# Optimization experiments

Hardware: AMD Instinct MI355X
Metric: run time of the kernel (lower is better)

## Reference

```python
import jax, jax.numpy as jnp
import numpy as np

CS = 128            # config.chunk_size
K = 8               # config.k + 1
EPS = 1e-6          # config.eps
L = K * CS          # extended_len = 1024


def setup_inputs() -> dict:
    key = jax.random.key(0)
    k1, k2 = jax.random.split(key)
    B, T, E = 2, 8192, 256
    x = jax.random.normal(k1, (B, T, E), dtype=jnp.float32)
    # xavier_normal_ on [CS, L]: std = sqrt(2 / (fan_in + fan_out))
    std = np.sqrt(2.0 / (CS + L)).astype(np.float32)
    down_proj = jax.random.normal(k2, (CS, L), dtype=jnp.float32) * std
    return {"x": x, "down_proj": down_proj}


def reference(x, down_proj):
    B, T, E = x.shape
    N = T // CS  # T chosen divisible by CS, so the pad branch is a no-op
    chunks = x.reshape(B, N, CS, E)

    # --- per-chunk retrieval scores (vectorized over the causal chunk loop) ---
    cn = chunks / (jnp.linalg.norm(chunks, axis=-1, keepdims=True) + EPS)
    # row-wise cosine sims between every pair of chunks: [B,N,N,CS,CS]
    sims = jnp.einsum('bice,bjde->bijcd', cn, cn)
    scores = sims.max(axis=-1).sum(axis=-1)              # [B,N,N]
    i_idx = jnp.arange(N)
    causal = i_idx[None, :] < i_idx[:, None]             # j < i allowed
    NEG = jnp.asarray(-1e9, x.dtype)
    scores = jnp.where(causal[None], scores, NEG)

    # --- topk selection, weights (num_sel_i = min(i, K-1)) ---
    vals, idx = jax.lax.top_k(scores, K - 1)             # descending, [B,N,K-1]
    num_sel = jnp.minimum(i_idx, K - 1)                  # [N]
    vmin_slot = jnp.clip(num_sel - 1, 0, K - 2)          # last valid slot = min of topk vals
    v_min = jnp.take_along_axis(vals, jnp.broadcast_to(vmin_slot[None, :, None], (B, N, 1)), axis=-1)
    slot = jnp.arange(K - 1)
    valid = slot[None, :] < num_sel[:, None]             # [N,K-1]
    w = jnp.where(valid[None], vals / (v_min + EPS), 0.0)  # [B,N,K-1]

    # --- weighted gather of selected chunks ---
    b_idx = jnp.arange(B)[:, None, None]
    sel = chunks[b_idx, idx]                             # [B,N,K-1,CS,E]
    weighted = sel * w[..., None, None]

    # --- left-pad to L: zeros occupy leftmost slots, then topk-ordered chunks, then cur ---
    shift = jnp.maximum(0, (K - 1) - i_idx)              # [N]
    src = jnp.clip(slot[None, :] - shift[:, None], 0, K - 2)   # [N,K-1]
    n_idx = jnp.arange(N)[None, :, None]
    arranged = weighted[b_idx, n_idx, src[None]]         # [B,N,K-1,CS,E]
    keep = slot[None, :] >= shift[:, None]
    arranged = jnp.where(keep[None, :, :, None, None], arranged, 0.0)

    ext = jnp.concatenate([arranged.reshape(B, N, (K - 1) * CS, E), chunks], axis=2)  # [B,N,L,E]
    # down_proj @ ext + x_chunks, then contract back to [B,T,E]
    out = jnp.einsum('cl,bnle->bnce', down_proj, ext) + chunks
    return out.reshape(B, N * CS, E)
```

## Files before the change

kernel.cpp:

```cpp
#include <hip/hip_runtime.h>
#include <hip/hip_bf16.h>

#define CS     128
#define EDIM   256
#define NBATCH 2
#define TLEN   8192
#define NCHUNK 64
#define LEXT   1024
#define KSEL   7

typedef __attribute__((ext_vector_type(8))) short   short8;
typedef __attribute__((ext_vector_type(4))) float   floatx4;

__device__ inline short bf16_of(float f) {
    __hip_bfloat16 h = __float2bfloat16(f);
    return *(short*)&h;
}
__device__ inline float f_of_bf16(short s) {
    __hip_bfloat16 h = *(__hip_bfloat16*)&s;
    return __bfloat162float(h);
}

__device__ inline void gl_lds16(const void* g, void* l) {
    __builtin_amdgcn_global_load_lds(
        (const __attribute__((address_space(1))) unsigned int*)g,
        (__attribute__((address_space(3))) unsigned int*)l, 16, 0, 0);
}

#define RAW_BAR() asm volatile("s_barrier" ::: "memory")

__global__ __launch_bounds__(256) void prep_kernel(const float* __restrict__ x,
                                                   const float* __restrict__ dp,
                                                   short* __restrict__ cn_hi,
                                                   short* __restrict__ cn_lo,
                                                   short* __restrict__ xt_hi,
                                                   short* __restrict__ dp_hi) {
    const int bx = blockIdx.x;
    if (bx >= 256) {
        int t = (bx - 256) * 256 + threadIdx.x;
#pragma unroll
        for (int u = 0; u < 16; ++u) {
            int idx = (t * 16 + u) * 4;
            float4 v = *(const float4*)(dp + idx);
            *(short4*)(dp_hi + idx) =
                make_short4(bf16_of(v.x), bf16_of(v.y), bf16_of(v.z), bf16_of(v.w));
        }
        return;
    }

    __shared__ float tile[64 * 257];
    const int b = bx >> 7, t0 = (bx & 127) * 64;
    const int tid = threadIdx.x;
    const int r = tid >> 2, q = tid & 3;

    const float* src = x + ((size_t)(b * TLEN + t0 + r)) * EDIM + q * 64;
    float* trow = &tile[r * 257 + q * 64];
    float s = 0.f;
#pragma unroll
    for (int u = 0; u < 16; ++u) {
        float4 v = *(const float4*)(src + u * 4);
        s += v.x * v.x + v.y * v.y + v.z * v.z + v.w * v.w;
        trow[u * 4 + 0] = v.x; trow[u * 4 + 1] = v.y;
        trow[u * 4 + 2] = v.z; trow[u * 4 + 3] = v.w;
    }
    s += __shfl_xor(s, 1);
    s += __shfl_xor(s, 2);
    const float rn = 1.0f / (sqrtf(s) + 1e-6f);

    short* ch = cn_hi + ((size_t)(b * TLEN + t0 + r)) * EDIM + q * 64;
    short* cl = cn_lo + ((size_t)(b * TLEN + t0 + r)) * EDIM + q * 64;
#pragma unroll
    for (int u = 0; u < 16; ++u) {
        short hs[4], ls[4];
#pragma unroll
        for (int k2 = 0; k2 < 4; ++k2) {
            float c = trow[u * 4 + k2] * rn;
            hs[k2] = bf16_of(c);
            ls[k2] = bf16_of(c - f_of_bf16(hs[k2]));
        }
        *(short4*)(ch + u * 4) = make_short4(hs[0], hs[1], hs[2], hs[3]);
        *(short4*)(cl + u * 4) = make_short4(ls[0], ls[1], ls[2], ls[3]);
    }
    __syncthreads();

    const int g16 = tid >> 4, tq = tid & 15;
#pragma unroll
    for (int it = 0; it < 16; ++it) {
        int e = g16 + it * 16;
        short hs2[4];
#pragma unroll
        for (int g = 0; g < 4; ++g)
            hs2[g] = bf16_of(tile[(tq * 4 + g) * 257 + e]);
        *(short4*)(xt_hi + ((size_t)(b * EDIM + e)) * TLEN + t0 + tq * 4)
            = make_short4(hs2[0], hs2[1], hs2[2], hs2[3]);
    }
}

__global__ __launch_bounds__(256) void scores_mfma(const short* __restrict__ cn_hi,
                                                   const short* __restrict__ cn_lo,
                                                   float* __restrict__ scores) {
    __shared__ short tiles[2][4][4096];
    double* red2   = (double*)&tiles[0][0][0];
    float*  redbuf = (float*)&tiles[0][0][8];

    const int p = blockIdx.x, b = blockIdx.y;
    int i = (int)((1.0f + sqrtf(1.0f + 8.0f * (float)p)) * 0.5f);
    while (i * (i - 1) / 2 > p) --i;
    while (i * (i + 1) / 2 <= p) ++i;
    const int j = p - i * (i - 1) / 2;

    const int tid  = threadIdx.x;
    const int w    = tid >> 6, lane = tid & 63;
    const int wr   = w >> 1, wc = w & 1;
    const int quad = lane >> 4, l15 = lane & 15;

    const short* sarr  = (w & 1) ? cn_lo : cn_hi;
    const size_t sbase = ((size_t)b * TLEN + ((w >> 1) ? j : i) * CS) * EDIM;
    const int rr  = lane >> 2;
    const int c16 = (lane & 3) * 8;
    const int csw = c16 ^ (((rr >> 1) & 3) * 8);
    const int q8  = (quad ^ ((l15 >> 1) & 3)) * 8;

    auto stage = [&](int ks, int bf) {
        const short* gsrc = sarr + sbase + ks * 32 + csw;
        short* ldst = &tiles[bf][w][0];
#pragma unroll
        for (int t = 0; t < 8; ++t)
            gl_lds16(gsrc + (size_t)(16 * t + rr) * EDIM, ldst + t * 512);
    };

    floatx4 acc[4][4];
#pragma unroll
    for (int rt = 0; rt < 4; ++rt)
#pragma unroll
        for (int ct = 0; ct < 4; ++ct) acc[rt][ct] = (floatx4){0.f, 0.f, 0.f, 0.f};

    stage(0, 0);
    int buf = 0;
    for (int ks = 0; ks < 8; ++ks) {
        if (ks < 7) {
            stage(ks + 1, buf ^ 1);
            asm volatile("s_waitcnt vmcnt(8)" ::: "memory");
        } else {
            asm volatile("s_waitcnt vmcnt(0)" ::: "memory");
        }
        RAW_BAR();

        short8 bh[4], bl[4];
#pragma unroll
        for (int ct = 0; ct < 4; ++ct) {
            int r = wc * 64 + ct * 16 + l15;
            bh[ct] = *(const short8*)&tiles[buf][2][r * 32 + q8];
            bl[ct] = *(const short8*)&tiles[buf][3][r * 32 + q8];
        }
        __builtin_amdgcn_s_setprio(1);
#pragma unroll
        for (int rt = 0; rt < 4; ++rt) {
            int r = wr * 64 + rt * 16 + l15;
            short8 ah = *(const short8*)&tiles[buf][0][r * 32 + q8];
            short8 al = *(const short8*)&tiles[buf][1][r * 32 + q8];
#pragma unroll
            for (int ct = 0; ct < 4; ++ct) {
                acc[rt][ct] = __builtin_amdgcn_mfma_f32_16x16x32_bf16(ah, bh[ct], acc[rt][ct], 0, 0, 0);
                acc[rt][ct] = __builtin_amdgcn_mfma_f32_16x16x32_bf16(ah, bl[ct], acc[rt][ct], 0, 0, 0);
                acc[rt][ct] = __builtin_amdgcn_mfma_f32_16x16x32_bf16(al, bh[ct], acc[rt][ct], 0, 0, 0);
            }
        }
        __builtin_amdgcn_s_setprio(0);
        RAW_BAR();
        buf ^= 1;
    }

#pragma unroll
    for (int rt = 0; rt < 4; ++rt) {
        float m[4];
#pragma unroll
        for (int reg = 0; reg < 4; ++reg) {
            float mm = acc[rt][0][reg];
#pragma unroll
            for (int ct = 1; ct < 4; ++ct) mm = fmaxf(mm, acc[rt][ct][reg]);
            m[reg] = mm;
        }
#pragma unroll
        for (int off = 1; off < 16; off <<= 1)
#pragma unroll
            for (int reg = 0; reg < 4; ++reg) m[reg] = fmaxf(m[reg], __shfl_xor(m[reg], off));
        if (l15 == 0) {
#pragma unroll
            for (int reg = 0; reg < 4; ++reg)
                redbuf[wc * 128 + wr * 64 + rt * 16 + quad * 4 + reg] = m[reg];
        }
    }
    __syncthreads();

    double part = 0.0;
    if (tid < 128) part = (double)fmaxf(redbuf[tid], redbuf[128 + tid]);
#pragma unroll
    for (int off = 1; off < 64; off <<= 1) part += __shfl_xor(part, off);
    if (lane == 0 && w < 2) red2[w] = part;
    __syncthreads();
    if (tid == 0) scores[(b * NCHUNK + i) * NCHUNK + j] = (float)(red2[0] + red2[1]);
}

__global__ __launch_bounds__(256) void out_mfma(const float* __restrict__ x,
                                                const short* __restrict__ dph,
                                                const short* __restrict__ xth,
                                                const float* __restrict__ scores,
                                                float* __restrict__ out) {
    __shared__ short As[2][128 * 32];
    __shared__ short Bs[2][64 * 32];
    __shared__ int   slist[8], sslot[8], snum;
    __shared__ float swei[8];

    const int eq = blockIdx.x, n = blockIdx.y, b = blockIdx.z;
    const int e0 = eq * 64;
    const int tid  = threadIdx.x;
    const int w    = tid >> 6, lane = tid & 63;
    const int wr   = w >> 1, wc = w & 1;
    const int quad = lane >> 4, l15 = lane & 15;
    const int rr   = lane >> 2;
    const int c16  = (lane & 3) * 8;
    const int csw  = c16 ^ (((rr >> 1) & 3) * 8);
    const int q8   = (quad ^ ((l15 >> 1) & 3)) * 8;

    if (w == 0) {
        const float* srow = scores + (b * NCHUNK + n) * NCHUNK;
        const int nsel = n < KSEL ? n : KSEL;
        float v = (lane < n) ? srow[lane] : -3.0e38f;
        float vals[KSEL];
        int   idxs[KSEL];
        for (int s2 = 0; s2 < nsel; ++s2) {
            float bv = v; int bi = lane;
#pragma unroll
            for (int off = 1; off < 64; off <<= 1) {
                float ov = __shfl_xor(bv, off);
                int   oi = __shfl_xor(bi, off);
                if (ov > bv || (ov == bv && oi < bi)) { bv = ov; bi = oi; }
            }
            vals[s2] = bv; idxs[s2] = bi;
            if (lane == bi) v = -3.0e38f;
        }
        if (lane == 0) {
            float vmin = (nsel > 0) ? vals[nsel - 1] : 0.0f;
            float inv  = 1.0f / (vmin + 1e-6f);
            int shift  = KSEL - nsel;
            int c = 0;
            for (int s2 = 0; s2 < 8; ++s2) {
                int jj; float ww;
                if (s2 < KSEL) {
                    int tt = s2 - shift;
                    if (tt >= 0) { jj = idxs[tt]; ww = vals[tt] * inv; }
                    else         { jj = -1;       ww = 0.0f; }
                } else { jj = n; ww = 1.0f; }
                if (jj >= 0) { slist[c] = jj; sslot[c] = s2; swei[c] = ww; ++c; }
            }
            snum = c;
        }
    }
    __syncthreads();
    const int NS = snum * 4;

    auto stage = [&](int st, int bf) {
        int sv = st >> 2, kk = st & 3;
        if (w < 2) {
            const short* gsrc = dph + (size_t)(sslot[sv] * 128 + kk * 32) + csw;
#pragma unroll
            for (int t = 0; t < 4; ++t)
                gl_lds16(gsrc + (size_t)(w * 64 + t * 16 + rr) * LEXT,
                         &As[bf][(w * 64 + t * 16) * 32]);
        } else {
            const short* gsrc = xth + ((size_t)(b * EDIM + e0)) * TLEN
                                + (size_t)(slist[sv] * CS + kk * 32) + csw;
#pragma unroll
            for (int t = 0; t < 2; ++t)
                gl_lds16(gsrc + (size_t)((w - 2) * 32 + t * 16 + rr) * TLEN,
                         &Bs[bf][((w - 2) * 32 + t * 16) * 32]);
        }
    };

    floatx4 accT[4][2], accP[4][2];
#pragma unroll
    for (int rt = 0; rt < 4; ++rt)
#pragma unroll
        for (int ct = 0; ct < 2; ++ct) accT[rt][ct] = (floatx4){0.f, 0.f, 0.f, 0.f};

    stage(0, 0);
    int buf = 0;
    for (int st = 0; st < NS; ++st) {
        if (st + 1 < NS) {
            stage(st + 1, buf ^ 1);
            if (w < 2) asm volatile("s_waitcnt vmcnt(4)" ::: "memory");
            else       asm volatile("s_waitcnt vmcnt(2)" ::: "memory");
        } else {
            asm volatile("s_waitcnt vmcnt(0)" ::: "memory");
        }
        RAW_BAR();

        if ((st & 3) == 0) {
#pragma unroll
            for (int rt = 0; rt < 4; ++rt)
#pragma unroll
                for (int ct = 0; ct < 2; ++ct) accP[rt][ct] = (floatx4){0.f, 0.f, 0.f, 0.f};
        }

        short8 bh[2];
#pragma unroll
        for (int ct = 0; ct < 2; ++ct) {
            int e = wc * 32 + ct * 16 + l15;
            bh[ct] = *(const short8*)&Bs[buf][e * 32 + q8];
        }
        __builtin_amdgcn_s_setprio(1);
#pragma unroll
        for (int rt = 0; rt < 4; ++rt) {
            int r = wr * 64 + rt * 16 + l15;
            short8 ah = *(const short8*)&As[buf][r * 32 + q8];
#pragma unroll
            for (int ct = 0; ct < 2; ++ct)
                accP[rt][ct] = __builtin_amdgcn_mfma_f32_16x16x32_bf16(ah, bh[ct], accP[rt][ct], 0, 0, 0);
        }
        __builtin_amdgcn_s_setprio(0);

        if ((st & 3) == 3) {
            float wcur = swei[st >> 2];
#pragma unroll
            for (int rt = 0; rt < 4; ++rt)
#pragma unroll
                for (int ct = 0; ct < 2; ++ct)
#pragma unroll
                    for (int reg = 0; reg < 4; ++reg)
                        accT[rt][ct][reg] += wcur * accP[rt][ct][reg];
        }
        RAW_BAR();
        buf ^= 1;
    }

#pragma unroll
    for (int rt = 0; rt < 4; ++rt)
#pragma unroll
        for (int ct = 0; ct < 2; ++ct) {
#pragma unroll
            for (int reg = 0; reg < 4; ++reg) {
                int row = wr * 64 + rt * 16 + quad * 4 + reg;
                int col = wc * 32 + ct * 16 + l15;
                size_t o = ((size_t)(b * TLEN + n * CS + row)) * EDIM + e0 + col;
                out[o] = accT[rt][ct][reg] + x[o];
            }
        }
}

extern "C" void kernel_launch(void* const* d_in, const int* in_sizes, int n_in,
                              void* d_out, int out_size, void* d_ws, size_t ws_size,
                              hipStream_t stream) {
    const float* x  = (const float*)d_in[0];
    const float* dp = (const float*)d_in[1];
    float* out = (float*)d_out;

    char* ws = (char*)d_ws;
    short* cn_hi  = (short*)(ws);
    short* cn_lo  = (short*)(ws + (8u << 20));
    short* xt_hi  = (short*)(ws + (16u << 20));
    short* dp_hi  = (short*)(ws + (24u << 20));
    float* scores = (float*)(ws + (25u << 20));

    prep_kernel <<<dim3(264), 256, 0, stream>>>(x, dp, cn_hi, cn_lo, xt_hi, dp_hi);
    scores_mfma <<<dim3(NCHUNK * (NCHUNK - 1) / 2, NBATCH), 256, 0, stream>>>(cn_hi, cn_lo, scores);
    out_mfma    <<<dim3(4, NCHUNK, NBATCH), 256, 0, stream>>>(x, dp_hi, xt_hi, scores, out);
}
```

Before: 203.2 us.

## Repack normalized chunks k-blocked, use 32x32 MFMA for scores, triple-buffer out GEMM

The prep kernel now writes the normalized hi/lo bf16 chunks in a k-slab-blocked layout, so the scores kernel can stage contiguous 16-wide K slices with fewer loads per stage. The scores kernel switches from 16x16x32 to 32x32x16 MFMA tiles, halves its LDS, and adds an occupancy hint of 4 blocks per SM. The row-max reduction is reworked to match the new accumulator layout. The output GEMM moves to a three-buffer pipeline that loads 64-wide K per stage with one barrier per step, cutting barrier and wait overhead at the cost of more LDS.

New measurement: 208.3 us. 2.5% more time.

```diff
diff --git a/kernel.cpp b/kernel.cpp
--- a/kernel.cpp
+++ b/kernel.cpp
@@ -9,8 +9,9 @@
 #define LEXT   1024
 #define KSEL   7
 
-typedef __attribute__((ext_vector_type(8))) short   short8;
-typedef __attribute__((ext_vector_type(4))) float   floatx4;
+typedef __attribute__((ext_vector_type(8)))  short short8;
+typedef __attribute__((ext_vector_type(4)))  float floatx4;
+typedef __attribute__((ext_vector_type(16))) float floatx16;
 
 __device__ inline short bf16_of(float f) {
     __hip_bfloat16 h = __float2bfloat16(f);
@@ -49,6 +50,7 @@
     }
 
     __shared__ float tile[64 * 257];
+    __shared__ float rnbuf[64];
     const int b = bx >> 7, t0 = (bx & 127) * 64;
     const int tid = threadIdx.x;
     const int r = tid >> 2, q = tid & 3;
@@ -66,21 +68,7 @@
     s += __shfl_xor(s, 1);
     s += __shfl_xor(s, 2);
     const float rn = 1.0f / (sqrtf(s) + 1e-6f);
-
-    short* ch = cn_hi + ((size_t)(b * TLEN + t0 + r)) * EDIM + q * 64;
-    short* cl = cn_lo + ((size_t)(b * TLEN + t0 + r)) * EDIM + q * 64;
-#pragma unroll
-    for (int u = 0; u < 16; ++u) {
-        short hs[4], ls[4];
-#pragma unroll
-        for (int k2 = 0; k2 < 4; ++k2) {
-            float c = trow[u * 4 + k2] * rn;
-            hs[k2] = bf16_of(c);
-            ls[k2] = bf16_of(c - f_of_bf16(hs[k2]));
-        }
-        *(short4*)(ch + u * 4) = make_short4(hs[0], hs[1], hs[2], hs[3]);
-        *(short4*)(cl + u * 4) = make_short4(ls[0], ls[1], ls[2], ls[3]);
-    }
+    if (q == 0) rnbuf[r] = rn;
     __syncthreads();
 
     const int g16 = tid >> 4, tq = tid & 15;
@@ -94,12 +82,35 @@
         *(short4*)(xt_hi + ((size_t)(b * EDIM + e)) * TLEN + t0 + tq * 4)
             = make_short4(hs2[0], hs2[1], hs2[2], hs2[3]);
     }
-}
-
-__global__ __launch_bounds__(256) void scores_mfma(const short* __restrict__ cn_hi,
-                                                   const short* __restrict__ cn_lo,
-                                                   float* __restrict__ scores) {
-    __shared__ short tiles[2][4][4096];
+
+    const int chunk = t0 >> 7, half = (t0 >> 6) & 1;
+    const size_t cbase = ((size_t)(b * 64 + chunk)) * 32768 + (size_t)half * 1024;
+    const int ks = tid >> 4, l16 = tid & 15;
+#pragma unroll
+    for (int rr = 0; rr < 4; ++rr) {
+        int lrow = rr * 16 + l16;
+        float rnv = rnbuf[lrow];
+        short8 h0, h1, l0, l1;
+#pragma unroll
+        for (int k2 = 0; k2 < 16; ++k2) {
+            float c = tile[lrow * 257 + ks * 16 + k2] * rnv;
+            short hh = bf16_of(c);
+            short ll = bf16_of(c - f_of_bf16(hh));
+            if (k2 < 8) { h0[k2] = hh; l0[k2] = ll; }
+            else        { h1[k2 - 8] = hh; l1[k2 - 8] = ll; }
+        }
+        size_t o = cbase + (size_t)ks * 2048 + (size_t)lrow * 16;
+        *(short8*)(cn_hi + o)     = h0;
+        *(short8*)(cn_hi + o + 8) = h1;
+        *(short8*)(cn_lo + o)     = l0;
+        *(short8*)(cn_lo + o + 8) = l1;
+    }
+}
+
+__global__ __launch_bounds__(256, 4) void scores_mfma(const short* __restrict__ cn_hi,
+                                                      const short* __restrict__ cn_lo,
+                                                      float* __restrict__ scores) {
+    __shared__ short tiles[2][4][2048];
     double* red2   = (double*)&tiles[0][0][0];
     float*  redbuf = (float*)&tiles[0][0][8];
 
@@ -112,58 +123,57 @@
     const int tid  = threadIdx.x;
     const int w    = tid >> 6, lane = tid & 63;
     const int wr   = w >> 1, wc = w & 1;
-    const int quad = lane >> 4, l15 = lane & 15;
+    const int hi   = lane >> 5, l31 = lane & 31;
 
     const short* sarr  = (w & 1) ? cn_lo : cn_hi;
-    const size_t sbase = ((size_t)b * TLEN + ((w >> 1) ? j : i) * CS) * EDIM;
-    const int rr  = lane >> 2;
-    const int c16 = (lane & 3) * 8;
-    const int csw = c16 ^ (((rr >> 1) & 3) * 8);
-    const int q8  = (quad ^ ((l15 >> 1) & 3)) * 8;
+    const size_t sbase = ((size_t)b * 64 + ((w >> 1) ? j : i)) * 32768;
+    const short* gsrc0 = sarr + sbase + lane * 8;
 
     auto stage = [&](int ks, int bf) {
-        const short* gsrc = sarr + sbase + ks * 32 + csw;
+        const short* g = gsrc0 + ks * 2048;
         short* ldst = &tiles[bf][w][0];
 #pragma unroll
-        for (int t = 0; t < 8; ++t)
-            gl_lds16(gsrc + (size_t)(16 * t + rr) * EDIM, ldst + t * 512);
+        for (int t = 0; t < 4; ++t)
+            gl_lds16(g + t * 512, ldst + t * 512);
     };
 
-    floatx4 acc[4][4];
-#pragma unroll
-    for (int rt = 0; rt < 4; ++rt)
-#pragma unroll
-        for (int ct = 0; ct < 4; ++ct) acc[rt][ct] = (floatx4){0.f, 0.f, 0.f, 0.f};
+    floatx16 acc[2][2];
+#pragma unroll
+    for (int rt = 0; rt < 2; ++rt)
+#pragma unroll
+        for (int ct = 0; ct < 2; ++ct)
+#pragma unroll
+            for (int reg = 0; reg < 16; ++reg) acc[rt][ct][reg] = 0.f;
 
     stage(0, 0);
     int buf = 0;
-    for (int ks = 0; ks < 8; ++ks) {
-        if (ks < 7) {
+    for (int ks = 0; ks < 16; ++ks) {
+        if (ks < 15) {
             stage(ks + 1, buf ^ 1);
-            asm volatile("s_waitcnt vmcnt(8)" ::: "memory");
+            asm volatile("s_waitcnt vmcnt(4)" ::: "memory");
         } else {
             asm volatile("s_waitcnt vmcnt(0)" ::: "memory");
         }
         RAW_BAR();
 
-        short8 bh[4], bl[4];
-#pragma unroll
-        for (int ct = 0; ct < 4; ++ct) {
-            int r = wc * 64 + ct * 16 + l15;
-            bh[ct] = *(const short8*)&tiles[buf][2][r * 32 + q8];
-            bl[ct] = *(const short8*)&tiles[buf][3][r * 32 + q8];
+        short8 bh[2], bl[2];
+#pragma unroll
+        for (int ct = 0; ct < 2; ++ct) {
+            int rb = wc * 64 + ct * 32 + l31;
+            bh[ct] = *(const short8*)&tiles[buf][2][rb * 16 + hi * 8];
+            bl[ct] = *(const short8*)&tiles[buf][3][rb * 16 + hi * 8];
         }
         __builtin_amdgcn_s_setprio(1);
 #pragma unroll
-        for (int rt = 0; rt < 4; ++rt) {
-            int r = wr * 64 + rt * 16 + l15;
-            short8 ah = *(const short8*)&tiles[buf][0][r * 32 + q8];
-            short8 al = *(const short8*)&tiles[buf][1][r * 32 + q8];
-#pragma unroll
-            for (int ct = 0; ct < 4; ++ct) {
-                acc[rt][ct] = __builtin_amdgcn_mfma_f32_16x16x32_bf16(ah, bh[ct], acc[rt][ct], 0, 0, 0);
-                acc[rt][ct] = __builtin_amdgcn_mfma_f32_16x16x32_bf16(ah, bl[ct], acc[rt][ct], 0, 0, 0);
-                acc[rt][ct] = __builtin_amdgcn_mfma_f32_16x16x32_bf16(al, bh[ct], acc[rt][ct], 0, 0, 0);
+        for (int rt = 0; rt < 2; ++rt) {
+            int ra = wr * 64 + rt * 32 + l31;
+            short8 ah = *(const short8*)&tiles[buf][0][ra * 16 + hi * 8];
+            short8 al = *(const short8*)&tiles[buf][1][ra * 16 + hi * 8];
+#pragma unroll
+            for (int ct = 0; ct < 2; ++ct) {
+                acc[rt][ct] = __builtin_amdgcn_mfma_f32_32x32x16_bf16(ah, bh[ct], acc[rt][ct], 0, 0, 0);
+                acc[rt][ct] = __builtin_amdgcn_mfma_f32_32x32x16_bf16(ah, bl[ct], acc[rt][ct], 0, 0, 0);
+                acc[rt][ct] = __builtin_amdgcn_mfma_f32_32x32x16_bf16(al, bh[ct], acc[rt][ct], 0, 0, 0);
             }
         }
         __builtin_amdgcn_s_setprio(0);
@@ -172,23 +182,22 @@
     }
 
 #pragma unroll
-    for (int rt = 0; rt < 4; ++rt) {
-        float m[4];
-#pragma unroll
-        for (int reg = 0; reg < 4; ++reg) {
-            float mm = acc[rt][0][reg];
-#pragma unroll
-            for (int ct = 1; ct < 4; ++ct) mm = fmaxf(mm, acc[rt][ct][reg]);
-            m[reg] = mm;
-        }
-#pragma unroll
-        for (int off = 1; off < 16; off <<= 1)
-#pragma unroll
-            for (int reg = 0; reg < 4; ++reg) m[reg] = fmaxf(m[reg], __shfl_xor(m[reg], off));
-        if (l15 == 0) {
-#pragma unroll
-            for (int reg = 0; reg < 4; ++reg)
-                redbuf[wc * 128 + wr * 64 + rt * 16 + quad * 4 + reg] = m[reg];
+    for (int rt = 0; rt < 2; ++rt) {
+        float m[16];
+#pragma unroll
+        for (int reg = 0; reg < 16; ++reg)
+            m[reg] = fmaxf(acc[rt][0][reg], acc[rt][1][reg]);
+#pragma unroll
+        for (int off = 1; off < 32; off <<= 1)
+#pragma unroll
+            for (int reg = 0; reg < 16; ++reg)
+                m[reg] = fmaxf(m[reg], __shfl_xor(m[reg], off));
+        if ((lane & 31) == 0) {
+#pragma unroll
+            for (int reg = 0; reg < 16; ++reg) {
+                int rowin = (reg & 3) + 8 * (reg >> 2) + 4 * hi;
+                redbuf[wc * 128 + wr * 64 + rt * 32 + rowin] = m[reg];
+            }
         }
     }
     __syncthreads();
@@ -207,8 +216,8 @@
                                                 const short* __restrict__ xth,
                                                 const float* __restrict__ scores,
                                                 float* __restrict__ out) {
-    __shared__ short As[2][128 * 32];
-    __shared__ short Bs[2][64 * 32];
+    __shared__ short As[3][2][128 * 32];
+    __shared__ short Bs[3][2][64 * 32];
     __shared__ int   slist[8], sslot[8], snum;
     __shared__ float swei[8];
 
@@ -258,23 +267,29 @@
         }
     }
     __syncthreads();
-    const int NS = snum * 4;
-
-    auto stage = [&](int st, int bf) {
-        int sv = st >> 2, kk = st & 3;
+    const int NT = snum * 2;
+
+    auto stage = [&](int st, int b3) {
+        int sv = st >> 1, kh = st & 1;
         if (w < 2) {
-            const short* gsrc = dph + (size_t)(sslot[sv] * 128 + kk * 32) + csw;
-#pragma unroll
-            for (int t = 0; t < 4; ++t)
-                gl_lds16(gsrc + (size_t)(w * 64 + t * 16 + rr) * LEXT,
-                         &As[bf][(w * 64 + t * 16) * 32]);
+#pragma unroll
+            for (int sub = 0; sub < 2; ++sub) {
+                const short* gsrc = dph + (size_t)(sslot[sv] * 128 + (kh * 2 + sub) * 32) + csw;
+#pragma unroll
+                for (int t = 0; t < 4; ++t)
+                    gl_lds16(gsrc + (size_t)(w * 64 + t * 16 + rr) * LEXT,
+                             &As[b3][sub][(w * 64 + t * 16) * 32]);
+            }
         } else {
-            const short* gsrc = xth + ((size_t)(b * EDIM + e0)) * TLEN
-                                + (size_t)(slist[sv] * CS + kk * 32) + csw;
-#pragma unroll
-            for (int t = 0; t < 2; ++t)
-                gl_lds16(gsrc + (size_t)((w - 2) * 32 + t * 16 + rr) * TLEN,
-                         &Bs[bf][((w - 2) * 32 + t * 16) * 32]);
+#pragma unroll
+            for (int sub = 0; sub < 2; ++sub) {
+                const short* gsrc = xth + ((size_t)(b * EDIM + e0)) * TLEN
+                                    + (size_t)(slist[sv] * CS + (kh * 2 + sub) * 32) + csw;
+#pragma unroll
+                for (int t = 0; t < 2; ++t)
+                    gl_lds16(gsrc + (size_t)((w - 2) * 32 + t * 16 + rr) * TLEN,
+                             &Bs[b3][sub][((w - 2) * 32 + t * 16) * 32]);
+            }
         }
     };
 
@@ -285,43 +300,43 @@
         for (int ct = 0; ct < 2; ++ct) accT[rt][ct] = (floatx4){0.f, 0.f, 0.f, 0.f};
 
     stage(0, 0);
-    int buf = 0;
-    for (int st = 0; st < NS; ++st) {
-        if (st + 1 < NS) {
-            stage(st + 1, buf ^ 1);
-            if (w < 2) asm volatile("s_waitcnt vmcnt(4)" ::: "memory");
-            else       asm volatile("s_waitcnt vmcnt(2)" ::: "memory");
-        } else {
-            asm volatile("s_waitcnt vmcnt(0)" ::: "memory");
-        }
+    if (NT > 1) stage(1, 1);
+    if (w < 2) asm volatile("s_waitcnt vmcnt(8)" ::: "memory");
+    else       asm volatile("s_waitcnt vmcnt(4)" ::: "memory");
+
+    int cur = 0;
+    for (int st = 0; st < NT; ++st) {
         RAW_BAR();
 
-        if ((st & 3) == 0) {
+        if ((st & 1) == 0) {
 #pragma unroll
             for (int rt = 0; rt < 4; ++rt)
 #pragma unroll
                 for (int ct = 0; ct < 2; ++ct) accP[rt][ct] = (floatx4){0.f, 0.f, 0.f, 0.f};
         }
 
-        short8 bh[2];
-#pragma unroll
-        for (int ct = 0; ct < 2; ++ct) {
-            int e = wc * 32 + ct * 16 + l15;
-            bh[ct] = *(const short8*)&Bs[buf][e * 32 + q8];
-        }
-        __builtin_amdgcn_s_setprio(1);
-#pragma unroll
-        for (int rt = 0; rt < 4; ++rt) {
-            int r = wr * 64 + rt * 16 + l15;
-            short8 ah = *(const short8*)&As[buf][r * 32 + q8];
-#pragma unroll
-            for (int ct = 0; ct < 2; ++ct)
-                accP[rt][ct] = __builtin_amdgcn_mfma_f32_16x16x32_bf16(ah, bh[ct], accP[rt][ct], 0, 0, 0);
-        }
-        __builtin_amdgcn_s_setprio(0);
-
-        if ((st & 3) == 3) {
-            float wcur = swei[st >> 2];
+#pragma unroll
+        for (int sub = 0; sub < 2; ++sub) {
+            short8 bh[2];
+#pragma unroll
+            for (int ct = 0; ct < 2; ++ct) {
+                int e = wc * 32 + ct * 16 + l15;
+                bh[ct] = *(const short8*)&Bs[cur][sub][e * 32 + q8];
+            }
+            __builtin_amdgcn_s_setprio(1);
+#pragma unroll
+            for (int rt = 0; rt < 4; ++rt) {
+                int r = wr * 64 + rt * 16 + l15;
+                short8 ah = *(const short8*)&As[cur][sub][r * 32 + q8];
+#pragma unroll
+                for (int ct = 0; ct < 2; ++ct)
+                    accP[rt][ct] = __builtin_amdgcn_mfma_f32_16x16x32_bf16(ah, bh[ct], accP[rt][ct], 0, 0, 0);
+            }
+            __builtin_amdgcn_s_setprio(0);
+        }
+
+        if ((st & 1) == 1) {
+            float wcur = swei[st >> 1];
 #pragma unroll
             for (int rt = 0; rt < 4; ++rt)
 #pragma unroll
@@ -330,8 +345,16 @@
                     for (int reg = 0; reg < 4; ++reg)
                         accT[rt][ct][reg] += wcur * accP[rt][ct][reg];
         }
-        RAW_BAR();
-        buf ^= 1;
+
+        if (st + 2 < NT) {
+            int tgt = cur ? cur - 1 : 2;
+            stage(st + 2, tgt);
+            if (w < 2) asm volatile("s_waitcnt vmcnt(8)" ::: "memory");
+            else       asm volatile("s_waitcnt vmcnt(4)" ::: "memory");
+        } else if (st + 1 < NT) {
+            asm volatile("s_waitcnt vmcnt(0)" ::: "memory");
+        }
+        cur = (cur == 2) ? 0 : cur + 1;
     }
 
 #pragma unroll
```

## Halve output tile width, load B operand directly from global, double grid

Applied to the files above, without the earlier changes.

The out_mfma kernel now covers 32 embedding columns per block instead of 64, which doubles the grid to 8x64x2 blocks. The B operand (transposed x chunks) is read straight from global memory into registers instead of being staged through LDS. All four waves now stage only the down_proj A tiles, in 64-wide K steps, and each wave owns 32 output rows. The aim is more parallelism and occupancy (launch bounds 4) and less LDS traffic, at the cost of reading down_proj twice as often across blocks and adding unstaged global latency on the B loads.

Measured after the change: 226.0 us. 1.11x slower.

```diff
diff --git a/kernel.cpp b/kernel.cpp
--- a/kernel.cpp
+++ b/kernel.cpp
@@ -202,21 +202,19 @@
     if (tid == 0) scores[(b * NCHUNK + i) * NCHUNK + j] = (float)(red2[0] + red2[1]);
 }
 
-__global__ __launch_bounds__(256) void out_mfma(const float* __restrict__ x,
-                                                const short* __restrict__ dph,
-                                                const short* __restrict__ xth,
-                                                const float* __restrict__ scores,
-                                                float* __restrict__ out) {
-    __shared__ short As[2][128 * 32];
-    __shared__ short Bs[2][64 * 32];
+__global__ __launch_bounds__(256, 4) void out_mfma(const float* __restrict__ x,
+                                                   const short* __restrict__ dph,
+                                                   const short* __restrict__ xth,
+                                                   const float* __restrict__ scores,
+                                                   float* __restrict__ out) {
+    __shared__ short As[2][2][128 * 32];
     __shared__ int   slist[8], sslot[8], snum;
     __shared__ float swei[8];
 
     const int eq = blockIdx.x, n = blockIdx.y, b = blockIdx.z;
-    const int e0 = eq * 64;
+    const int e0 = eq * 32;
     const int tid  = threadIdx.x;
     const int w    = tid >> 6, lane = tid & 63;
-    const int wr   = w >> 1, wc = w & 1;
     const int quad = lane >> 4, l15 = lane & 15;
     const int rr   = lane >> 2;
     const int c16  = (lane & 3) * 8;
@@ -258,72 +256,70 @@
         }
     }
     __syncthreads();
-    const int NS = snum * 4;
-
+    const int NT = snum * 2;
+
+    const int sub_w = w >> 1, p_w = w & 1;
     auto stage = [&](int st, int bf) {
-        int sv = st >> 2, kk = st & 3;
-        if (w < 2) {
-            const short* gsrc = dph + (size_t)(sslot[sv] * 128 + kk * 32) + csw;
-#pragma unroll
-            for (int t = 0; t < 4; ++t)
-                gl_lds16(gsrc + (size_t)(w * 64 + t * 16 + rr) * LEXT,
-                         &As[bf][(w * 64 + t * 16) * 32]);
-        } else {
-            const short* gsrc = xth + ((size_t)(b * EDIM + e0)) * TLEN
-                                + (size_t)(slist[sv] * CS + kk * 32) + csw;
-#pragma unroll
-            for (int t = 0; t < 2; ++t)
-                gl_lds16(gsrc + (size_t)((w - 2) * 32 + t * 16 + rr) * TLEN,
-                         &Bs[bf][((w - 2) * 32 + t * 16) * 32]);
-        }
+        int sv = st >> 1, kh = st & 1;
+        const short* gsrc = dph + (size_t)(sslot[sv] * 128 + kh * 64 + sub_w * 32) + csw;
+#pragma unroll
+        for (int t = 0; t < 4; ++t)
+            gl_lds16(gsrc + (size_t)(p_w * 64 + t * 16 + rr) * LEXT,
+                     &As[bf][sub_w][(p_w * 64 + t * 16) * 32]);
     };
 
-    floatx4 accT[4][2], accP[4][2];
-#pragma unroll
-    for (int rt = 0; rt < 4; ++rt)
+    floatx4 accT[2][2], accP[2][2];
+#pragma unroll
+    for (int rt = 0; rt < 2; ++rt)
 #pragma unroll
         for (int ct = 0; ct < 2; ++ct) accT[rt][ct] = (floatx4){0.f, 0.f, 0.f, 0.f};
+
+    const short* xbase = xth + ((size_t)(b * EDIM + e0 + l15)) * TLEN + quad * 8;
 
     stage(0, 0);
     int buf = 0;
-    for (int st = 0; st < NS; ++st) {
-        if (st + 1 < NS) {
+    for (int st = 0; st < NT; ++st) {
+        if (st + 1 < NT) {
             stage(st + 1, buf ^ 1);
-            if (w < 2) asm volatile("s_waitcnt vmcnt(4)" ::: "memory");
-            else       asm volatile("s_waitcnt vmcnt(2)" ::: "memory");
+            asm volatile("s_waitcnt vmcnt(4)" ::: "memory");
         } else {
             asm volatile("s_waitcnt vmcnt(0)" ::: "memory");
         }
         RAW_BAR();
 
-        if ((st & 3) == 0) {
-#pragma unroll
-            for (int rt = 0; rt < 4; ++rt)
+        const int sv = st >> 1, kh = st & 1;
+        const size_t kbase = (size_t)(slist[sv] * CS + kh * 64);
+
+        if (kh == 0) {
+#pragma unroll
+            for (int rt = 0; rt < 2; ++rt)
 #pragma unroll
                 for (int ct = 0; ct < 2; ++ct) accP[rt][ct] = (floatx4){0.f, 0.f, 0.f, 0.f};
         }
 
-        short8 bh[2];
-#pragma unroll
-        for (int ct = 0; ct < 2; ++ct) {
-            int e = wc * 32 + ct * 16 + l15;
-            bh[ct] = *(const short8*)&Bs[buf][e * 32 + q8];
-        }
-        __builtin_amdgcn_s_setprio(1);
-#pragma unroll
-        for (int rt = 0; rt < 4; ++rt) {
-            int r = wr * 64 + rt * 16 + l15;
-            short8 ah = *(const short8*)&As[buf][r * 32 + q8];
+#pragma unroll
+        for (int sub = 0; sub < 2; ++sub) {
+            short8 bh[2];
 #pragma unroll
             for (int ct = 0; ct < 2; ++ct)
-                accP[rt][ct] = __builtin_amdgcn_mfma_f32_16x16x32_bf16(ah, bh[ct], accP[rt][ct], 0, 0, 0);
-        }
-        __builtin_amdgcn_s_setprio(0);
-
-        if ((st & 3) == 3) {
-            float wcur = swei[st >> 2];
-#pragma unroll
-            for (int rt = 0; rt < 4; ++rt)
+                bh[ct] = *(const short8*)(xbase + (size_t)(ct * 16) * TLEN
+                                          + kbase + sub * 32);
+            __builtin_amdgcn_s_setprio(1);
+#pragma unroll
+            for (int rt = 0; rt < 2; ++rt) {
+                int r = w * 32 + rt * 16 + l15;
+                short8 ah = *(const short8*)&As[buf][sub][r * 32 + q8];
+#pragma unroll
+                for (int ct = 0; ct < 2; ++ct)
+                    accP[rt][ct] = __builtin_amdgcn_mfma_f32_16x16x32_bf16(ah, bh[ct], accP[rt][ct], 0, 0, 0);
+            }
+            __builtin_amdgcn_s_setprio(0);
+        }
+
+        if (kh == 1) {
+            float wcur = swei[sv];
+#pragma unroll
+            for (int rt = 0; rt < 2; ++rt)
 #pragma unroll
                 for (int ct = 0; ct < 2; ++ct)
 #pragma unroll
@@ -335,13 +331,13 @@
     }
 
 #pragma unroll
-    for (int rt = 0; rt < 4; ++rt)
+    for (int rt = 0; rt < 2; ++rt)
 #pragma unroll
         for (int ct = 0; ct < 2; ++ct) {
 #pragma unroll
             for (int reg = 0; reg < 4; ++reg) {
-                int row = wr * 64 + rt * 16 + quad * 4 + reg;
-                int col = wc * 32 + ct * 16 + l15;
+                int row = w * 32 + rt * 16 + quad * 4 + reg;
+                int col = ct * 16 + l15;
                 size_t o = ((size_t)(b * TLEN + n * CS + row)) * EDIM + e0 + col;
                 out[o] = accT[rt][ct][reg] + x[o];
             }
@@ -364,5 +360,5 @@
 
     prep_kernel <<<dim3(264), 256, 0, stream>>>(x, dp, cn_hi, cn_lo, xt_hi, dp_hi);
     scores_mfma <<<dim3(NCHUNK * (NCHUNK - 1) / 2, NBATCH), 256, 0, stream>>>(cn_hi, cn_lo, scores);
-    out_mfma    <<<dim3(4, NCHUNK, NBATCH), 256, 0, stream>>>(x, dp_hi, xt_hi, scores, out);
-}
+    out_mfma    <<<dim3(8, NCHUNK, NBATCH), 256, 0, stream>>>(x, dp_hi, xt_hi, scores, out);
+}
```

## Use eight waves in scores kernel and triple-buffer out kernel pipeline

Applied to the files above, without the earlier changes.

The scores kernel now runs 512 threads per block: eight waves each own a 64x32 output sub-tile, and each pair of waves stages half of one operand tile. This raises the number of waves available to hide latency, at the cost of a four-way max reduction. The out kernel now loads 64-wide K slices into a three-deep LDS ring and prefetches two stages ahead, with one barrier per iteration instead of two. That ring raises LDS use to about 72KB per block, which may limit how many blocks fit on a CU.

New measurement: 203.9 us. Within noise of the previous version (+0.3%).

```diff
diff --git a/kernel.cpp b/kernel.cpp
--- a/kernel.cpp
+++ b/kernel.cpp
@@ -96,7 +96,7 @@
     }
 }
 
-__global__ __launch_bounds__(256) void scores_mfma(const short* __restrict__ cn_hi,
+__global__ __launch_bounds__(512) void scores_mfma(const short* __restrict__ cn_hi,
                                                    const short* __restrict__ cn_lo,
                                                    float* __restrict__ scores) {
     __shared__ short tiles[2][4][4096];
@@ -111,11 +111,12 @@
 
     const int tid  = threadIdx.x;
     const int w    = tid >> 6, lane = tid & 63;
-    const int wr   = w >> 1, wc = w & 1;
+    const int wr   = w >> 2, wc = w & 3;
     const int quad = lane >> 4, l15 = lane & 15;
 
-    const short* sarr  = (w & 1) ? cn_lo : cn_hi;
-    const size_t sbase = ((size_t)b * TLEN + ((w >> 1) ? j : i) * CS) * EDIM;
+    const int tt = w >> 1, hh = w & 1;
+    const short* sarr  = (tt & 1) ? cn_lo : cn_hi;
+    const size_t sbase = ((size_t)b * TLEN + ((tt >> 1) ? j : i) * CS) * EDIM;
     const int rr  = lane >> 2;
     const int c16 = (lane & 3) * 8;
     const int csw = c16 ^ (((rr >> 1) & 3) * 8);
@@ -123,33 +124,33 @@
 
     auto stage = [&](int ks, int bf) {
         const short* gsrc = sarr + sbase + ks * 32 + csw;
-        short* ldst = &tiles[bf][w][0];
-#pragma unroll
-        for (int t = 0; t < 8; ++t)
-            gl_lds16(gsrc + (size_t)(16 * t + rr) * EDIM, ldst + t * 512);
+        short* ldst = &tiles[bf][tt][hh * 2048];
+#pragma unroll
+        for (int t = 0; t < 4; ++t)
+            gl_lds16(gsrc + (size_t)(hh * 64 + 16 * t + rr) * EDIM, ldst + t * 512);
     };
 
-    floatx4 acc[4][4];
+    floatx4 acc[4][2];
 #pragma unroll
     for (int rt = 0; rt < 4; ++rt)
 #pragma unroll
-        for (int ct = 0; ct < 4; ++ct) acc[rt][ct] = (floatx4){0.f, 0.f, 0.f, 0.f};
+        for (int ct = 0; ct < 2; ++ct) acc[rt][ct] = (floatx4){0.f, 0.f, 0.f, 0.f};
 
     stage(0, 0);
     int buf = 0;
     for (int ks = 0; ks < 8; ++ks) {
         if (ks < 7) {
             stage(ks + 1, buf ^ 1);
-            asm volatile("s_waitcnt vmcnt(8)" ::: "memory");
+            asm volatile("s_waitcnt vmcnt(4)" ::: "memory");
         } else {
             asm volatile("s_waitcnt vmcnt(0)" ::: "memory");
         }
         RAW_BAR();
 
-        short8 bh[4], bl[4];
-#pragma unroll
-        for (int ct = 0; ct < 4; ++ct) {
-            int r = wc * 64 + ct * 16 + l15;
+        short8 bh[2], bl[2];
+#pragma unroll
+        for (int ct = 0; ct < 2; ++ct) {
+            int r = wc * 32 + ct * 16 + l15;
             bh[ct] = *(const short8*)&tiles[buf][2][r * 32 + q8];
             bl[ct] = *(const short8*)&tiles[buf][3][r * 32 + q8];
         }
@@ -160,7 +161,7 @@
             short8 ah = *(const short8*)&tiles[buf][0][r * 32 + q8];
             short8 al = *(const short8*)&tiles[buf][1][r * 32 + q8];
 #pragma unroll
-            for (int ct = 0; ct < 4; ++ct) {
+            for (int ct = 0; ct < 2; ++ct) {
                 acc[rt][ct] = __builtin_amdgcn_mfma_f32_16x16x32_bf16(ah, bh[ct], acc[rt][ct], 0, 0, 0);
                 acc[rt][ct] = __builtin_amdgcn_mfma_f32_16x16x32_bf16(ah, bl[ct], acc[rt][ct], 0, 0, 0);
                 acc[rt][ct] = __builtin_amdgcn_mfma_f32_16x16x32_bf16(al, bh[ct], acc[rt][ct], 0, 0, 0);
@@ -175,12 +176,8 @@
     for (int rt = 0; rt < 4; ++rt) {
         float m[4];
 #pragma unroll
-        for (int reg = 0; reg < 4; ++reg) {
-            float mm = acc[rt][0][reg];
-#pragma unroll
-            for (int ct = 1; ct < 4; ++ct) mm = fmaxf(mm, acc[rt][ct][reg]);
-            m[reg] = mm;
-        }
+        for (int reg = 0; reg < 4; ++reg)
+            m[reg] = fmaxf(acc[rt][0][reg], acc[rt][1][reg]);
 #pragma unroll
         for (int off = 1; off < 16; off <<= 1)
 #pragma unroll
@@ -194,7 +191,9 @@
     __syncthreads();
 
     double part = 0.0;
-    if (tid < 128) part = (double)fmaxf(redbuf[tid], redbuf[128 + tid]);
+    if (tid < 128)
+        part = (double)fmaxf(fmaxf(redbuf[tid], redbuf[128 + tid]),
+                             fmaxf(redbuf[256 + tid], redbuf[384 + tid]));
 #pragma unroll
     for (int off = 1; off < 64; off <<= 1) part += __shfl_xor(part, off);
     if (lane == 0 && w < 2) red2[w] = part;
@@ -207,8 +206,8 @@
                                                 const short* __restrict__ xth,
                                                 const float* __restrict__ scores,
                                                 float* __restrict__ out) {
-    __shared__ short As[2][128 * 32];
-    __shared__ short Bs[2][64 * 32];
+    __shared__ short As[3][2][128 * 32];
+    __shared__ short Bs[3][2][64 * 32];
     __shared__ int   slist[8], sslot[8], snum;
     __shared__ float swei[8];
 
@@ -258,23 +257,29 @@
         }
     }
     __syncthreads();
-    const int NS = snum * 4;
-
-    auto stage = [&](int st, int bf) {
-        int sv = st >> 2, kk = st & 3;
+    const int NT = snum * 2;
+
+    auto stage = [&](int st, int b3) {
+        int sv = st >> 1, kh = st & 1;
         if (w < 2) {
-            const short* gsrc = dph + (size_t)(sslot[sv] * 128 + kk * 32) + csw;
-#pragma unroll
-            for (int t = 0; t < 4; ++t)
-                gl_lds16(gsrc + (size_t)(w * 64 + t * 16 + rr) * LEXT,
-                         &As[bf][(w * 64 + t * 16) * 32]);
+#pragma unroll
+            for (int sub = 0; sub < 2; ++sub) {
+                const short* gsrc = dph + (size_t)(sslot[sv] * 128 + (kh * 2 + sub) * 32) + csw;
+#pragma unroll
+                for (int t = 0; t < 4; ++t)
+                    gl_lds16(gsrc + (size_t)(w * 64 + t * 16 + rr) * LEXT,
+                             &As[b3][sub][(w * 64 + t * 16) * 32]);
+            }
         } else {
-            const short* gsrc = xth + ((size_t)(b * EDIM + e0)) * TLEN
-                                + (size_t)(slist[sv] * CS + kk * 32) + csw;
-#pragma unroll
-            for (int t = 0; t < 2; ++t)
-                gl_lds16(gsrc + (size_t)((w - 2) * 32 + t * 16 + rr) * TLEN,
-                         &Bs[bf][((w - 2) * 32 + t * 16) * 32]);
+#pragma unroll
+            for (int sub = 0; sub < 2; ++sub) {
+                const short* gsrc = xth + ((size_t)(b * EDIM + e0)) * TLEN
+                                    + (size_t)(slist[sv] * CS + (kh * 2 + sub) * 32) + csw;
+#pragma unroll
+                for (int t = 0; t < 2; ++t)
+                    gl_lds16(gsrc + (size_t)((w - 2) * 32 + t * 16 + rr) * TLEN,
+                             &Bs[b3][sub][((w - 2) * 32 + t * 16) * 32]);
+            }
         }
     };
 
@@ -285,43 +290,43 @@
         for (int ct = 0; ct < 2; ++ct) accT[rt][ct] = (floatx4){0.f, 0.f, 0.f, 0.f};
 
     stage(0, 0);
-    int buf = 0;
-    for (int st = 0; st < NS; ++st) {
-        if (st + 1 < NS) {
-            stage(st + 1, buf ^ 1);
-            if (w < 2) asm volatile("s_waitcnt vmcnt(4)" ::: "memory");
-            else       asm volatile("s_waitcnt vmcnt(2)" ::: "memory");
-        } else {
-            asm volatile("s_waitcnt vmcnt(0)" ::: "memory");
-        }
+    if (NT > 1) stage(1, 1);
+    if (w < 2) asm volatile("s_waitcnt vmcnt(8)" ::: "memory");
+    else       asm volatile("s_waitcnt vmcnt(4)" ::: "memory");
+
+    int cur = 0;
+    for (int st = 0; st < NT; ++st) {
         RAW_BAR();
 
-        if ((st & 3) == 0) {
+        if ((st & 1) == 0) {
 #pragma unroll
             for (int rt = 0; rt < 4; ++rt)
 #pragma unroll
                 for (int ct = 0; ct < 2; ++ct) accP[rt][ct] = (floatx4){0.f, 0.f, 0.f, 0.f};
         }
 
-        short8 bh[2];
-#pragma unroll
-        for (int ct = 0; ct < 2; ++ct) {
-            int e = wc * 32 + ct * 16 + l15;
-            bh[ct] = *(const short8*)&Bs[buf][e * 32 + q8];
-        }
-        __builtin_amdgcn_s_setprio(1);
-#pragma unroll
-        for (int rt = 0; rt < 4; ++rt) {
-            int r = wr * 64 + rt * 16 + l15;
-            short8 ah = *(const short8*)&As[buf][r * 32 + q8];
-#pragma unroll
-            for (int ct = 0; ct < 2; ++ct)
-                accP[rt][ct] = __builtin_amdgcn_mfma_f32_16x16x32_bf16(ah, bh[ct], accP[rt][ct], 0, 0, 0);
-        }
-        __builtin_amdgcn_s_setprio(0);
-
-        if ((st & 3) == 3) {
-            float wcur = swei[st >> 2];
+#pragma unroll
+        for (int sub = 0; sub < 2; ++sub) {
+            short8 bh[2];
+#pragma unroll
+            for (int ct = 0; ct < 2; ++ct) {
+                int e = wc * 32 + ct * 16 + l15;
+                bh[ct] = *(const short8*)&Bs[cur][sub][e * 32 + q8];
+            }
+            __builtin_amdgcn_s_setprio(1);
+#pragma unroll
+            for (int rt = 0; rt < 4; ++rt) {
+                int r = wr * 64 + rt * 16 + l15;
+                short8 ah = *(const short8*)&As[cur][sub][r * 32 + q8];
+#pragma unroll
+                for (int ct = 0; ct < 2; ++ct)
+                    accP[rt][ct] = __builtin_amdgcn_mfma_f32_16x16x32_bf16(ah, bh[ct], accP[rt][ct], 0, 0, 0);
+            }
+            __builtin_amdgcn_s_setprio(0);
+        }
+
+        if ((st & 1) == 1) {
+            float wcur = swei[st >> 1];
 #pragma unroll
             for (int rt = 0; rt < 4; ++rt)
 #pragma unroll
@@ -330,8 +335,16 @@
                     for (int reg = 0; reg < 4; ++reg)
                         accT[rt][ct][reg] += wcur * accP[rt][ct][reg];
         }
-        RAW_BAR();
-        buf ^= 1;
+
+        if (st + 2 < NT) {
+            int tgt = cur ? cur - 1 : 2;
+            stage(st + 2, tgt);
+            if (w < 2) asm volatile("s_waitcnt vmcnt(8)" ::: "memory");
+            else       asm volatile("s_waitcnt vmcnt(4)" ::: "memory");
+        } else if (st + 1 < NT) {
+            asm volatile("s_waitcnt vmcnt(0)" ::: "memory");
+        }
+        cur = (cur == 2) ? 0 : cur + 1;
     }
 
 #pragma unroll
@@ -363,6 +376,6 @@
     float* scores = (float*)(ws + (25u << 20));
 
     prep_kernel <<<dim3(264), 256, 0, stream>>>(x, dp, cn_hi, cn_lo, xt_hi, dp_hi);
-    scores_mfma <<<dim3(NCHUNK * (NCHUNK - 1) / 2, NBATCH), 256, 0, stream>>>(cn_hi, cn_lo, scores);
+    scores_mfma <<<dim3(NCHUNK * (NCHUNK - 1) / 2, NBATCH), 512, 0, stream>>>(cn_hi, cn_lo, scores);
     out_mfma    <<<dim3(4, NCHUNK, NBATCH), 256, 0, stream>>>(x, dp_hi, xt_hi, scores, out);
 }
```
